# Kernel optimization log

Measured on AMD Instinct MI355X. Metric: run time of the kernel, lower is better.

Reference implementation:

```python
import jax, jax.numpy as jnp
import numpy as np

# dims
B, LP, CIN, AUX = 8, 1024, 64, 32
COUT, OUT_LEN = 64, 512
DM, DI, NS, PH, NH = 1024, 2048, 16, 64, 32  # d_model, d_inner, d_state, headdim, n_heads
NL, PATCH, KPRE, KCONV = 4, 8, 5, 4
GG, KH, CHUNK = 8, 2048, 64  # kan grid, kan hidden, chunk_size
DIN = 2 * DI + 2 * NS + NH   # in_proj output: z, xBC, dt
CONV_DIM = DI + 2 * NS


def _conv1d(x, w, b, stride, pad_l, pad_r, groups=1):
    # x: [B, C, L], w: [O, I/groups, K]
    y = jax.lax.conv_general_dilated(x, w, (stride,), [(pad_l, pad_r)],
                                     dimension_numbers=("NCH", "OIH", "NCH"),
                                     feature_group_count=groups)
    return y + b[None, :, None]


def _rmsnorm(x, w):
    return x * jax.lax.rsqrt(jnp.mean(x * x, axis=-1, keepdims=True) + 1e-5) * w


def _mamba(u, in_w, conv_w, conv_b, A_log, Dh, dt_bias, out_w):
    # Mamba2-style selective SSM block (bias-free projections, causal depthwise conv).
    Bs, L, _ = u.shape
    zxbcdt = jnp.einsum("bld,ed->ble", u, in_w)  # [B,L,DIN]
    z = zxbcdt[..., :DI]
    xBC = zxbcdt[..., DI:DI + CONV_DIM]
    dt = jax.nn.softplus(zxbcdt[..., DI + CONV_DIM:] + dt_bias)  # [B,L,NH]
    xBC = jax.nn.silu(_conv1d(xBC.transpose(0, 2, 1), conv_w, conv_b, 1, KCONV - 1, 0,
                              groups=CONV_DIM)).transpose(0, 2, 1)
    xh = xBC[..., :DI].reshape(Bs, L, NH, PH)
    Bm = xBC[..., DI:DI + NS]   # [B,L,NS]
    Cm = xBC[..., DI + NS:]     # [B,L,NS]
    dA = jnp.exp(-jnp.exp(A_log) * dt)  # [B,L,NH]

    def step(s, t):
        x_t, B_t, C_t, dA_t, dt_t = t
        s = s * dA_t[:, :, None, None] + jnp.einsum("bhp,bn,bh->bhpn", x_t, B_t, dt_t)
        return s, jnp.einsum("bhpn,bn->bhp", s, C_t)

    s0 = jnp.zeros((Bs, NH, PH, NS), u.dtype)
    xs = (xh.transpose(1, 0, 2, 3), Bm.transpose(1, 0, 2), Cm.transpose(1, 0, 2),
          dA.transpose(1, 0, 2), dt.transpose(1, 0, 2))
    _, ys = jax.lax.scan(step, s0, xs)  # ys: [L,B,NH,PH]
    y = ys.transpose(1, 0, 2, 3) + xh * Dh[None, None, :, None]
    y = y.reshape(Bs, L, DI) * jax.nn.silu(z)
    return jnp.einsum("ble,de->bld", y, out_w)


def _kan(x, log_bw, base_w, base_b, spline_w):
    # Gaussian-basis KAN layer: base Linear + spline Linear over RBF expansion.
    grid = jnp.linspace(-2.0, 2.0, GG)
    bw = jnp.exp(log_bw)[None] + 1e-6                 # [1,in,1]
    basis = jnp.exp(-((x[..., None] - grid[None, None, :]) ** 2) / (2.0 * bw * bw))
    return x @ base_w.T + base_b + basis.reshape(x.shape[0], -1) @ spline_w.T


def setup_inputs() -> dict:
    ks = iter(jax.random.split(jax.random.key(0), 64))
    nrm = lambda shape, s=0.02: jax.random.normal(next(ks), shape, jnp.float32) * s
    inp = {"x_prefix": jax.random.normal(next(ks), (B, LP, CIN), jnp.float32),
           "y_aux": jax.random.normal(next(ks), (B, AUX), jnp.float32),
           "pre_conv_w": nrm((DM, CIN, KPRE), 0.1), "pre_conv_b": jnp.zeros((DM,)),
           "patch_w": nrm((DM, DM, PATCH), 0.05), "patch_b": jnp.zeros((DM,))}
    for pre in ("fwd", "bwd"):
        inp[pre + "_norm_w"] = jnp.ones((NL, DM))
        inp[pre + "_in_w"] = nrm((NL, DIN, DM))
        inp[pre + "_conv_w"] = nrm((NL, CONV_DIM, 1, KCONV), 0.1)
        inp[pre + "_conv_b"] = jnp.zeros((NL, CONV_DIM))
        inp[pre + "_A_log"] = jnp.zeros((NL, NH))
        inp[pre + "_D"] = jnp.ones((NL, NH))
        inp[pre + "_dt_bias"] = nrm((NL, NH), 0.5)
        inp[pre + "_out_w"] = nrm((NL, DM, DI))
    inp.update(aux_w=nrm((DM, AUX)), aux_b=jnp.zeros((DM,)),
               kan1_log_bw=jnp.zeros((3 * DM, 1)), kan1_base_w=nrm((KH, 3 * DM)),
               kan1_base_b=jnp.zeros((KH,)), kan1_spline_w=nrm((KH, 3 * DM * GG), 0.005),
               kan2_log_bw=jnp.zeros((KH, 1)), kan2_base_w=nrm((DM, KH)),
               kan2_base_b=jnp.zeros((DM,)), kan2_spline_w=nrm((DM, KH * GG), 0.005),
               shared_w=nrm((DM, DM)), shared_b=jnp.zeros((DM,)),
               heads_w=nrm((COUT, OUT_LEN, DM)), heads_b=jnp.zeros((COUT, OUT_LEN)))
    return inp


def reference(x_prefix, y_aux, pre_conv_w, pre_conv_b, patch_w, patch_b,
              fwd_norm_w, fwd_in_w, fwd_conv_w, fwd_conv_b, fwd_A_log, fwd_D, fwd_dt_bias, fwd_out_w,
              bwd_norm_w, bwd_in_w, bwd_conv_w, bwd_conv_b, bwd_A_log, bwd_D, bwd_dt_bias, bwd_out_w,
              aux_w, aux_b, kan1_log_bw, kan1_base_w, kan1_base_b, kan1_spline_w,
              kan2_log_bw, kan2_base_w, kan2_base_b, kan2_spline_w,
              shared_w, shared_b, heads_w, heads_b):
    # encode_prefix
    x = jax.nn.silu(_conv1d(x_prefix.transpose(0, 2, 1), pre_conv_w, pre_conv_b, 1, KPRE // 2, KPRE // 2))
    x = _conv1d(x, patch_w, patch_b, PATCH, 0, 0).transpose(0, 2, 1)  # [B, 128, DM]
    rem = x.shape[1] % CHUNK
    if rem:
        x = jnp.pad(x, ((0, 0), (0, CHUNK - rem), (0, 0)))
    h_f, h_b = x, x[:, ::-1]
    for i in range(NL):
        h_f = h_f + _mamba(_rmsnorm(h_f, fwd_norm_w[i]), fwd_in_w[i], fwd_conv_w[i], fwd_conv_b[i],
                           fwd_A_log[i], fwd_D[i], fwd_dt_bias[i], fwd_out_w[i])
        h_b = h_b + _mamba(_rmsnorm(h_b, bwd_norm_w[i]), bwd_in_w[i], bwd_conv_w[i], bwd_conv_b[i],
                           bwd_A_log[i], bwd_D[i], bwd_dt_bias[i], bwd_out_w[i])
    ctx = jnp.concatenate([h_f.mean(1), h_b[:, ::-1].mean(1)], axis=-1)  # [B, 2*DM]
    # fusion + heads
    aux = jax.nn.silu(y_aux @ aux_w.T + aux_b)
    fused = jnp.concatenate([ctx, aux], axis=-1)  # [B, 3*DM]
    fused = jax.nn.silu(_kan(fused, kan1_log_bw, kan1_base_w, kan1_base_b, kan1_spline_w))
    fused = jax.nn.silu(_kan(fused, kan2_log_bw, kan2_base_w, kan2_base_b, kan2_spline_w))
    fused = jax.nn.silu(fused @ shared_w.T + shared_b)
    # all channel heads fused into one batched GEMM: [B, OUT_LEN, COUT]
    return jnp.einsum("bd,cld->blc", fused, heads_w) + heads_b.T[None]
```

## Files before the change

kernel.cpp:

```cpp
#include <hip/hip_runtime.h>
#include <hip/hip_bf16.h>
#include <math.h>

#define B_    8
#define LP_   1024
#define CIN_  64
#define DM_   1024
#define DI_   2048
#define NS_   16
#define PH_   64
#define NH_   32
#define NL_   4
#define GG_   8
#define KH_   2048
#define DIN_  4160
#define NPAD_ 4224
#define CONVD_ 2080
#define L_    128
#define R_    1024
#define OUTL_ 512
#define COUT_ 64

typedef __bf16 bf16x8 __attribute__((ext_vector_type(8)));
typedef float f32x4 __attribute__((ext_vector_type(4)));
typedef unsigned short ushort;

__device__ __forceinline__ float silu_f(float x) { return x / (1.0f + expf(-x)); }

__device__ __forceinline__ ushort f2bu(float x) {
    union { __hip_bfloat16 h; ushort u; } c; c.h = __float2bfloat16(x); return c.u;
}
__device__ __forceinline__ float bu2f(ushort u) {
    union { ushort u; __hip_bfloat16 h; } c; c.u = u; return __bfloat162float(c.h);
}

__device__ __forceinline__ void gload_lds16(const void* g, void* l) {
    __builtin_amdgcn_global_load_lds((const __attribute__((address_space(1))) unsigned int*)g,
                                     (__attribute__((address_space(3))) unsigned int*)l, 16, 0, 0);
}

__device__ __forceinline__ float merge2(float a, float b, int mask, int lane) {
    float x = (lane & mask) ? b : a;
    float y = (lane & mask) ? a : b;
    return x + __shfl_xor(y, mask);
}
__device__ __forceinline__ float reduce8(float* a, int lane) {
    float c0 = merge2(a[0], a[1], 1, lane);
    float c1 = merge2(a[2], a[3], 1, lane);
    float c2 = merge2(a[4], a[5], 1, lane);
    float c3 = merge2(a[6], a[7], 1, lane);
    float d0 = merge2(c0, c1, 2, lane);
    float d1 = merge2(c2, c3, 2, lane);
    float e  = merge2(d0, d1, 4, lane);
    e += __shfl_xor(e, 8);
    e += __shfl_xor(e, 16);
    e += __shfl_xor(e, 32);
    return e;
}

__global__ __launch_bounds__(256) void k_pre_im2col(const float* __restrict__ xp, __hip_bfloat16* __restrict__ out) {
    size_t idx = (size_t)blockIdx.x * 256 + threadIdx.x;
    if (idx >= (size_t)8192 * 320) return;
    int kk = (int)(idx % 320); size_t r = idx / 320;
    int l = (int)(r & 1023); int b = (int)(r >> 10);
    int kp = kk >> 6, c = kk & 63;
    int lp = l + kp - 2;
    float v = 0.f;
    if (lp >= 0 && lp < LP_) v = xp[((size_t)b * LP_ + lp) * CIN_ + c];
    out[idx] = __float2bfloat16(v);
}

__global__ __launch_bounds__(256) void k_wpre_T(const float* __restrict__ w, __hip_bfloat16* __restrict__ out) {
    int idx = blockIdx.x * 256 + threadIdx.x;
    if (idx >= DM_ * 320) return;
    int d = idx / 320, kk = idx % 320;
    int kp = kk >> 6, c = kk & 63;
    out[idx] = __float2bfloat16(w[(d * CIN_ + c) * 5 + kp]);
}

__global__ __launch_bounds__(256) void k_wpatch_T(const float* __restrict__ w, __hip_bfloat16* __restrict__ out) {
    size_t idx = (size_t)blockIdx.x * 256 + threadIdx.x;
    if (idx >= (size_t)DM_ * 8192) return;
    int d = (int)(idx >> 13); int kk = (int)(idx & 8191);
    int kp = kk >> 10, din = kk & 1023;
    out[idx] = __float2bfloat16(w[((size_t)d << 13) + din * 8 + kp]);
}

#define CVT_IN_T4  1081344
#define CVT_OUT_T4 524288
__global__ __launch_bounds__(256) void k_cvt_layer(const float* __restrict__ in0, const float* __restrict__ in1,
                                                   const float* __restrict__ o0, const float* __restrict__ o1,
                                                   __hip_bfloat16* __restrict__ wBB, __hip_bfloat16* __restrict__ wOB) {
    int i = blockIdx.x * 256 + threadIdx.x;
    int dir = 0;
    if (i >= CVT_IN_T4 + CVT_OUT_T4) { dir = 1; i -= CVT_IN_T4 + CVT_OUT_T4; }
    const float* inw = dir ? in1 : in0;
    const float* outw = dir ? o1 : o0;
    if (i < CVT_IN_T4) {
        int idx = i * 4; int row = idx >> 10;
        __hip_bfloat16* dst = wBB + (size_t)dir * NPAD_ * 1024 + idx;
        if (row < DIN_) {
            float4 v = *(const float4*)(inw + idx);
            dst[0] = __float2bfloat16(v.x); dst[1] = __float2bfloat16(v.y);
            dst[2] = __float2bfloat16(v.z); dst[3] = __float2bfloat16(v.w);
        } else {
            dst[0] = __float2bfloat16(0.f); dst[1] = __float2bfloat16(0.f);
            dst[2] = __float2bfloat16(0.f); dst[3] = __float2bfloat16(0.f);
        }
    } else {
        int idx = (i - CVT_IN_T4) * 4;
        __hip_bfloat16* dst = wOB + (size_t)dir * 1024 * 2048 + idx;
        float4 v = *(const float4*)(outw + idx);
        dst[0] = __float2bfloat16(v.x); dst[1] = __float2bfloat16(v.y);
        dst[2] = __float2bfloat16(v.z); dst[3] = __float2bfloat16(v.w);
    }
}

template<int BM, int BN>
__global__ __launch_bounds__(256) void k_gemm_mfma(
    const ushort* __restrict__ A, const ushort* __restrict__ B,
    const float* __restrict__ bias, const float* __restrict__ resid,
    float* __restrict__ Cf, __hip_bfloat16* __restrict__ Cb,
    int Kc, int ldk, int ldc, int Nstore, int act, long sA, long sB, long sC)
{
    constexpr int BK = 32;
    constexpr int WM = BM / 2, WN = BN / 2;
    constexpr int MR = WM / 16, NR = WN / 16;
    constexpr int ACH = BM * 4, BCH = BN * 4;
    __shared__ ushort sAs[2][BM * BK];
    __shared__ ushort sBs[2][BN * BK];
    int tid = threadIdx.x;
    int lane = tid & 63, w = tid >> 6;
    int wr = w >> 1, wc = w & 1;
    int z = blockIdx.z;
    int m0 = blockIdx.y * BM, n0 = blockIdx.x * BN;
    int kbase = (act == 2) ? z * Kc : 0;
    const ushort* Az = A + (size_t)(act == 2 ? 0 : z) * sA + kbase;
    const ushort* Bz = B + (size_t)(act == 2 ? 0 : z) * sB + kbase;

    auto STAGE = [&](int buf, int k0) {
        #pragma unroll
        for (int c = tid; c < ACH; c += 256) {
            int row = c >> 2, col = (c & 3) * 8;
            gload_lds16(Az + (size_t)(m0 + row) * ldk + k0 + col, (char*)&sAs[buf][0] + c * 16);
        }
        #pragma unroll
        for (int c = tid; c < BCH; c += 256) {
            int row = c >> 2, col = (c & 3) * 8;
            gload_lds16(Bz + (size_t)(n0 + row) * ldk + k0 + col, (char*)&sBs[buf][0] + c * 16);
        }
    };

    f32x4 acc[MR][NR] = {};
    const int NT = Kc / BK;
    STAGE(0, 0);
    __syncthreads();
    int cur = 0;
    for (int t = 0; t < NT; ++t) {
        if (t + 1 < NT) STAGE(cur ^ 1, (t + 1) * BK);
        bf16x8 af[MR], bfr[NR];
        #pragma unroll
        for (int m = 0; m < MR; ++m)
            af[m] = *(const bf16x8*)&sAs[cur][(wr * WM + m * 16 + (lane & 15)) * BK + (lane >> 4) * 8];
        #pragma unroll
        for (int n = 0; n < NR; ++n)
            bfr[n] = *(const bf16x8*)&sBs[cur][(wc * WN + n * 16 + (lane & 15)) * BK + (lane >> 4) * 8];
        #pragma unroll
        for (int m = 0; m < MR; ++m)
            #pragma unroll
            for (int n = 0; n < NR; ++n)
                acc[m][n] = __builtin_amdgcn_mfma_f32_16x16x32_bf16(af[m], bfr[n], acc[m][n], 0, 0, 0);
        __syncthreads();
        cur ^= 1;
    }
    const float* residz = resid ? resid + (size_t)z * sC : nullptr;
    float* Cfz = Cf ? Cf + (size_t)z * sC : nullptr;
    __hip_bfloat16* Cbz = Cb ? Cb + (size_t)z * sC : nullptr;
    #pragma unroll
    for (int m = 0; m < MR; ++m) {
        int row = m0 + wr * WM + m * 16 + (lane >> 4) * 4;
        #pragma unroll
        for (int n = 0; n < NR; ++n) {
            int col = n0 + wc * WN + n * 16 + (lane & 15);
            if (col < Nstore) {
                float bv = (bias && act != 2) ? bias[col] : 0.f;
                #pragma unroll
                for (int j = 0; j < 4; ++j) {
                    float v = acc[m][n][j] + bv;
                    if (residz) v += residz[(size_t)(row + j) * ldc + col];
                    if (act == 1) v = silu_f(v);
                    if (Cbz) Cbz[(size_t)(row + j) * ldc + col] = __float2bfloat16(v);
                    else     Cfz[(size_t)(row + j) * ldc + col] = v;
                }
            }
        }
    }
}

__global__ __launch_bounds__(256) void k_patch_fin(const float* __restrict__ part, const float* __restrict__ bias,
                                                   float* __restrict__ hf, float* __restrict__ hb) {
    int i4 = blockIdx.x * 256 + threadIdx.x;
    int idx = i4 * 4;
    int r = idx >> 10, c = idx & 1023;
    float4 v = *(const float4*)(part + idx);
    float4 v1 = *(const float4*)(part + 1048576 + idx);
    float4 v2 = *(const float4*)(part + 2097152 + idx);
    float4 v3 = *(const float4*)(part + 3145728 + idx);
    float4 bv = *(const float4*)(bias + c);
    float4 o;
    o.x = v.x + v1.x + v2.x + v3.x + bv.x;
    o.y = v.y + v1.y + v2.y + v3.y + bv.y;
    o.z = v.z + v1.z + v2.z + v3.z + bv.z;
    o.w = v.w + v1.w + v2.w + v3.w + bv.w;
    *(float4*)(hf + idx) = o;
    *(float4*)(hb + (((size_t)(r ^ 127)) << 10) + c) = o;
}

__global__ __launch_bounds__(256) void k_rmsnorm(const float* __restrict__ h, const float* __restrict__ w0,
                                                 const float* __restrict__ w1, __hip_bfloat16* __restrict__ u) {
    int r = blockIdx.x; int t = threadIdx.x;
    const float* w = (r >> 10) ? w1 : w0;
    const float* row = h + (size_t)r * DM_;
    float v[4]; float ss = 0.f;
    #pragma unroll
    for (int i = 0; i < 4; ++i) { v[i] = row[t + 256 * i]; ss += v[i] * v[i]; }
    #pragma unroll
    for (int o = 32; o; o >>= 1) ss += __shfl_xor(ss, o);
    __shared__ float sred[4];
    if ((t & 63) == 0) sred[t >> 6] = ss;
    __syncthreads();
    float tot = sred[0] + sred[1] + sred[2] + sred[3];
    float scale = rsqrtf(tot * (1.0f / DM_) + 1e-5f);
    #pragma unroll
    for (int i = 0; i < 4; ++i)
        u[(size_t)r * DM_ + t + 256 * i] = __float2bfloat16(v[i] * scale * w[t + 256 * i]);
}

__global__ __launch_bounds__(256) void k_dwconv(const __hip_bfloat16* __restrict__ zx,
                                                const float* __restrict__ cw0, const float* __restrict__ cw1,
                                                const float* __restrict__ cb0, const float* __restrict__ cb1,
                                                __hip_bfloat16* __restrict__ xbc) {
    int idx = blockIdx.x * 256 + threadIdx.x;
    if (idx >= 2048 * 520) return;
    int c4 = idx % 520; int r = idx / 520;
    int dir = r >> 10, rl = r & 1023, l = rl & 127;
    const float* cw = (dir ? cw1 : cw0) + c4 * 16;
    const float* cb = (dir ? cb1 : cb0) + c4 * 4;
    const __hip_bfloat16* zxd = zx + (size_t)dir * 1024 * DIN_;
    float4 acc = *(const float4*)cb;
    #pragma unroll
    for (int k = 0; k < 4; ++k) {
        int lp = l - 3 + k;
        if (lp >= 0) {
            ushort4 raw = *(const ushort4*)(zxd + (size_t)(rl - l + lp) * DIN_ + DI_ + c4 * 4);
            acc.x += bu2f(raw.x) * cw[0 * 4 + k];
            acc.y += bu2f(raw.y) * cw[1 * 4 + k];
            acc.z += bu2f(raw.z) * cw[2 * 4 + k];
            acc.w += bu2f(raw.w) * cw[3 * 4 + k];
        }
    }
    ushort4 o;
    o.x = f2bu(silu_f(acc.x)); o.y = f2bu(silu_f(acc.y));
    o.z = f2bu(silu_f(acc.z)); o.w = f2bu(silu_f(acc.w));
    *(ushort4*)(xbc + (size_t)dir * 1024 * CONVD_ + (size_t)rl * CONVD_ + c4 * 4) = o;
}

__global__ __launch_bounds__(256) void k_scan(const __hip_bfloat16* __restrict__ xbc, const __hip_bfloat16* __restrict__ zx,
                                              const float* __restrict__ dtb0, const float* __restrict__ dtb1,
                                              const float* __restrict__ al0, const float* __restrict__ al1,
                                              const float* __restrict__ D0, const float* __restrict__ D1,
                                              __hip_bfloat16* __restrict__ ys) {
    __shared__ float xs[L_ * PH_];
    __shared__ float Bsh[L_ * NS_];
    __shared__ float Csh[L_ * NS_];
    __shared__ float dts[L_];
    __shared__ float dAs[L_];
    int bx = blockIdx.x;
    int dir = bx >> 8, b = (bx >> 5) & 7, h = bx & 31;
    const __hip_bfloat16* xbcd = xbc + (size_t)dir * 1024 * CONVD_;
    const __hip_bfloat16* zxd  = zx  + (size_t)dir * 1024 * DIN_;
    const float* dt_bias = dir ? dtb1 : dtb0;
    const float* A_log   = dir ? al1 : al0;
    const float* Dh      = dir ? D1 : D0;
    __hip_bfloat16* ysd  = ys + (size_t)dir * 1024 * DI_;
    int t = threadIdx.x;
    for (int i = t; i < L_ * PH_; i += 256) {
        int l = i >> 6, p = i & 63;
        xs[i] = __bfloat162float(xbcd[((size_t)(b * L_ + l)) * CONVD_ + h * PH_ + p]);
    }
    for (int i = t; i < L_ * NS_; i += 256) {
        int l = i >> 4, n = i & 15;
        Bsh[i] = __bfloat162float(xbcd[((size_t)(b * L_ + l)) * CONVD_ + DI_ + n]);
        Csh[i] = __bfloat162float(xbcd[((size_t)(b * L_ + l)) * CONVD_ + DI_ + NS_ + n]);
    }
    if (t < L_) {
        float v = __bfloat162float(zxd[((size_t)(b * L_ + t)) * DIN_ + 4128 + h]) + dt_bias[h];
        float sp = v > 20.f ? v : log1pf(expf(v));
        dts[t] = sp;
        dAs[t] = expf(-expf(A_log[h]) * sp);
    }
    __syncthreads();
    int p = t >> 2, n0 = (t & 3) * 4;
    float Dv = Dh[h];
    float s0 = 0.f, s1 = 0.f, s2 = 0.f, s3 = 0.f;
    for (int l = 0; l < L_; ++l) {
        float x = xs[l * 64 + p];
        float dAv = dAs[l];
        float xdt = x * dts[l];
        s0 = s0 * dAv + xdt * Bsh[l * 16 + n0 + 0];
        s1 = s1 * dAv + xdt * Bsh[l * 16 + n0 + 1];
        s2 = s2 * dAv + xdt * Bsh[l * 16 + n0 + 2];
        s3 = s3 * dAv + xdt * Bsh[l * 16 + n0 + 3];
        float cp = s0 * Csh[l * 16 + n0 + 0] + s1 * Csh[l * 16 + n0 + 1]
                 + s2 * Csh[l * 16 + n0 + 2] + s3 * Csh[l * 16 + n0 + 3];
        cp += __shfl_xor(cp, 1);
        cp += __shfl_xor(cp, 2);
        if ((t & 3) == 0) xs[l * 64 + p] = cp + x * Dv;
    }
    __syncthreads();
    for (int i = t; i < L_ * PH_; i += 256) {
        int l = i >> 6, pp = i & 63;
        float z = __bfloat162float(zxd[((size_t)(b * L_ + l)) * DIN_ + h * PH_ + pp]);
        ysd[((size_t)(b * L_ + l)) * DI_ + h * PH_ + pp] = __float2bfloat16(xs[i] * silu_f(z));
    }
}

__global__ __launch_bounds__(256) void k_meanctx(const float* __restrict__ hf, const float* __restrict__ hb,
                                                 float* __restrict__ fused) {
    int b = blockIdx.x, t = threadIdx.x;
    int d = t * 4;
    float4 sf = {0,0,0,0}, sb = {0,0,0,0};
    for (int l = 0; l < L_; ++l) {
        float4 a = *(const float4*)(hf + ((size_t)b * L_ + l) * DM_ + d);
        float4 c = *(const float4*)(hb + ((size_t)b * L_ + l) * DM_ + d);
        sf.x += a.x; sf.y += a.y; sf.z += a.z; sf.w += a.w;
        sb.x += c.x; sb.y += c.y; sb.z += c.z; sb.w += c.w;
    }
    const float s = 1.f / L_;
    float4 o1 = {sf.x*s, sf.y*s, sf.z*s, sf.w*s};
    float4 o2 = {sb.x*s, sb.y*s, sb.z*s, sb.w*s};
    *(float4*)(fused + b * 3072 + d) = o1;
    *(float4*)(fused + b * 3072 + DM_ + d) = o2;
}

__global__ __launch_bounds__(256) void k_aux(const float* __restrict__ y_aux, const float* __restrict__ aux_w,
                                             const float* __restrict__ aux_b, float* __restrict__ fused) {
    int j = blockIdx.x * 256 + threadIdx.x;
    if (j >= DM_) return;
    for (int b = 0; b < B_; ++b) {
        float acc = aux_b[j];
        for (int a = 0; a < 32; ++a) acc += y_aux[b * 32 + a] * aux_w[j * 32 + a];
        fused[b * 3072 + 2 * DM_ + j] = silu_f(acc);
    }
}

__global__ __launch_bounds__(256) void k_basis(const float* __restrict__ x, const float* __restrict__ log_bw,
                                               float* __restrict__ basis, int Din) {
    int idx = blockIdx.x * 256 + threadIdx.x;
    if (idx >= 8 * Din) return;
    int d = idx % Din;
    float xv = x[idx];
    float bw = expf(log_bw[d]) + 1e-6f;
    float inv = 1.0f / (2.0f * bw * bw);
    #pragma unroll
    for (int g = 0; g < GG_; ++g) {
        float gg = -2.0f + g * (4.0f / 7.0f);
        float df = xv - gg;
        basis[(size_t)idx * GG_ + g] = expf(-df * df * inv);
    }
}

template<int MODE>
__global__ __launch_bounds__(256) void k_dotl(const float* __restrict__ W, const float* __restrict__ X,
                                              const float* __restrict__ bias, float* __restrict__ out,
                                              int K, int Dout, int ldx, int nch, int chOff) {
    __shared__ float sX[8][1024];
    int ch = blockIdx.y;
    int k0 = ch * 1024;
    int tid = threadIdx.x;
    for (int i = tid; i < 2048; i += 256) {
        int b = i >> 8, kk = (i & 255) * 4;
        *(float4*)&sX[b][kk] = *(const float4*)(X + (size_t)b * ldx + k0 + kk);
    }
    __syncthreads();
    int wv = tid >> 6, lane = tid & 63;
    int rowBase = blockIdx.x * 32 + wv * 8;
    for (int j = 0; j < 8; ++j) {
        int row = rowBase + j;
        const float* wr = W + (size_t)row * K + k0;
        float acc[8] = {};
        #pragma unroll
        for (int it = 0; it < 4; ++it) {
            int k = it * 256 + lane * 4;
            float4 wvv = *(const float4*)(wr + k);
            #pragma unroll
            for (int b = 0; b < 8; ++b) {
                float4 xv = *(const float4*)&sX[b][k];
                acc[b] += wvv.x * xv.x + wvv.y * xv.y + wvv.z * xv.z + wvv.w * xv.w;
            }
        }
        float e = reduce8(acc, lane);
        if (lane < 8) {
            if (MODE == 0) {
                out[((size_t)row * nch + chOff + ch) * 8 + lane] = e;
            } else if (MODE == 1) {
                out[(size_t)lane * Dout + row] = silu_f(e + bias[row]);
            } else {
                int c = row >> 9, l = row & 511;
                out[((size_t)lane * OUTL_ + l) * COUT_ + c] = e + bias[row];
            }
        }
    }
}

template<int NCH>
__global__ __launch_bounds__(256) void k_dot_fin(const float* __restrict__ partial, const float* __restrict__ base_b,
                                                 float* __restrict__ out, int Dout) {
    int row = blockIdx.x * 256 + threadIdx.x;
    if (row >= Dout) return;
    float bb = base_b[row];
    #pragma unroll
    for (int b = 0; b < 8; ++b) {
        float s = bb;
        #pragma unroll
        for (int c = 0; c < NCH; ++c) s += partial[((size_t)row * NCH + c) * 8 + b];
        out[(size_t)b * Dout + row] = silu_f(s);
    }
}

extern "C" void kernel_launch(void* const* d_in, const int* in_sizes, int n_in,
                              void* d_out, int out_size, void* d_ws, size_t ws_size,
                              hipStream_t stream) {
    const float* x_prefix = (const float*)d_in[0];
    const float* y_aux    = (const float*)d_in[1];
    const float* pre_w    = (const float*)d_in[2];
    const float* pre_b    = (const float*)d_in[3];
    const float* patch_w  = (const float*)d_in[4];
    const float* patch_b  = (const float*)d_in[5];
    const float* norm_w[2] = {(const float*)d_in[6],  (const float*)d_in[14]};
    const float* in_w[2]   = {(const float*)d_in[7],  (const float*)d_in[15]};
    const float* conv_w[2] = {(const float*)d_in[8],  (const float*)d_in[16]};
    const float* conv_b[2] = {(const float*)d_in[9],  (const float*)d_in[17]};
    const float* A_log[2]  = {(const float*)d_in[10], (const float*)d_in[18]};
    const float* Dvec[2]   = {(const float*)d_in[11], (const float*)d_in[19]};
    const float* dt_b[2]   = {(const float*)d_in[12], (const float*)d_in[20]};
    const float* out_w[2]  = {(const float*)d_in[13], (const float*)d_in[21]};
    const float* aux_w = (const float*)d_in[22];
    const float* aux_b = (const float*)d_in[23];
    const float* k1_lbw = (const float*)d_in[24];
    const float* k1_bw  = (const float*)d_in[25];
    const float* k1_bb  = (const float*)d_in[26];
    const float* k1_sw  = (const float*)d_in[27];
    const float* k2_lbw = (const float*)d_in[28];
    const float* k2_bw  = (const float*)d_in[29];
    const float* k2_bb  = (const float*)d_in[30];
    const float* k2_sw  = (const float*)d_in[31];
    const float* sh_w = (const float*)d_in[32];
    const float* sh_b = (const float*)d_in[33];
    const float* hw   = (const float*)d_in[34];
    const float* hbias= (const float*)d_in[35];
    float* ws = (float*)d_ws;
    float* out = (float*)d_out;

    const size_t o_ApreB   = 0;
    const size_t o_wpreTB  = 1310720;
    const size_t o_x1B     = 1474560;
    const size_t o_wpatchTB= 5668864;
    const size_t o_ppart   = 9863168;
    const size_t o_uB   = 0;
    const size_t o_zxB  = 1048576;
    const size_t o_xbcB = 5308416;
    const size_t o_ysB  = 7438336;
    const size_t o_wBB  = 9535488;
    const size_t o_wOB  = 13860864;
    const size_t o_hf   = 15958016;
    const size_t o_hb   = 17006592;
    const size_t total_f = 18055168;
    const size_t o_f1   = 0;
    const size_t o_bas1 = 24576;
    const size_t o_k1   = 221184;
    const size_t o_bas2 = 237568;
    const size_t o_k2   = 368640;
    const size_t o_f4   = 376832;
    const size_t o_part = 385024;
    if (ws_size < total_f * sizeof(float)) return;

    __hip_bfloat16* ApreB   = (__hip_bfloat16*)(ws + o_ApreB);
    __hip_bfloat16* wpreTB  = (__hip_bfloat16*)(ws + o_wpreTB);
    __hip_bfloat16* x1B     = (__hip_bfloat16*)(ws + o_x1B);
    __hip_bfloat16* wpatchTB= (__hip_bfloat16*)(ws + o_wpatchTB);
    __hip_bfloat16* uB      = (__hip_bfloat16*)(ws + o_uB);
    __hip_bfloat16* zxB     = (__hip_bfloat16*)(ws + o_zxB);
    __hip_bfloat16* xbcB    = (__hip_bfloat16*)(ws + o_xbcB);
    __hip_bfloat16* ysB     = (__hip_bfloat16*)(ws + o_ysB);
    __hip_bfloat16* wBB     = (__hip_bfloat16*)(ws + o_wBB);
    __hip_bfloat16* wOB     = (__hip_bfloat16*)(ws + o_wOB);
    float* hf = ws + o_hf;
    float* hb = ws + o_hb;

    k_wpre_T<<<1280, 256, 0, stream>>>(pre_w, wpreTB);
    k_wpatch_T<<<32768, 256, 0, stream>>>(patch_w, wpatchTB);
    k_pre_im2col<<<10240, 256, 0, stream>>>(x_prefix, ApreB);
    k_gemm_mfma<128,128><<<dim3(8, 64, 1), 256, 0, stream>>>(
        (const ushort*)ApreB, (const ushort*)wpreTB, pre_b, nullptr, nullptr, x1B,
        320, 320, 1024, 1024, 1, 0, 0, 0);
    k_gemm_mfma<64,64><<<dim3(16, 16, 4), 256, 0, stream>>>(
        (const ushort*)x1B, (const ushort*)wpatchTB, nullptr, nullptr, ws + o_ppart, nullptr,
        2048, 8192, 1024, 1024, 2, 0, 0, (long)1024 * 1024);
    k_patch_fin<<<1024, 256, 0, stream>>>(ws + o_ppart, patch_b, hf, hb);

    for (int i = 0; i < NL_; ++i) {
        k_rmsnorm<<<2048, 256, 0, stream>>>(hf, norm_w[0] + (size_t)i * DM_, norm_w[1] + (size_t)i * DM_, uB);
        k_cvt_layer<<<12544, 256, 0, stream>>>(
            in_w[0] + (size_t)i * DIN_ * DM_, in_w[1] + (size_t)i * DIN_ * DM_,
            out_w[0] + (size_t)i * DM_ * DI_, out_w[1] + (size_t)i * DM_ * DI_, wBB, wOB);
        k_gemm_mfma<128,128><<<dim3(33, 8, 2), 256, 0, stream>>>(
            (const ushort*)uB, (const ushort*)wBB, nullptr, nullptr, nullptr, zxB,
            1024, 1024, DIN_, DIN_, 0, (long)1024 * 1024, (long)NPAD_ * 1024, (long)1024 * DIN_);
        k_dwconv<<<4160, 256, 0, stream>>>(zxB,
            conv_w[0] + (size_t)i * CONVD_ * 4, conv_w[1] + (size_t)i * CONVD_ * 4,
            conv_b[0] + (size_t)i * CONVD_, conv_b[1] + (size_t)i * CONVD_, xbcB);
        k_scan<<<512, 256, 0, stream>>>(xbcB, zxB,
            dt_b[0] + i * NH_, dt_b[1] + i * NH_, A_log[0] + i * NH_, A_log[1] + i * NH_,
            Dvec[0] + i * NH_, Dvec[1] + i * NH_, ysB);
        k_gemm_mfma<64,64><<<dim3(16, 16, 2), 256, 0, stream>>>(
            (const ushort*)ysB, (const ushort*)wOB, nullptr, hf, hf, nullptr,
            2048, 2048, 1024, 1024, 0, (long)1024 * 2048, (long)1024 * 2048, (long)1024 * 1024);
    }

    k_meanctx<<<8, 256, 0, stream>>>(hf, hb, ws + o_f1);
    k_aux<<<4, 256, 0, stream>>>(y_aux, aux_w, aux_b, ws + o_f1);
    k_basis<<<96, 256, 0, stream>>>(ws + o_f1, k1_lbw, ws + o_bas1, 3072);
    k_dotl<0><<<dim3(64, 24), 256, 0, stream>>>(k1_sw, ws + o_bas1, nullptr, ws + o_part, 24576, 2048, 24576, 27, 0);
    k_dotl<0><<<dim3(64, 3),  256, 0, stream>>>(k1_bw, ws + o_f1,   nullptr, ws + o_part, 3072,  2048, 3072,  27, 24);
    k_dot_fin<27><<<8, 256, 0, stream>>>(ws + o_part, k1_bb, ws + o_k1, 2048);
    k_basis<<<64, 256, 0, stream>>>(ws + o_k1, k2_lbw, ws + o_bas2, 2048);
    k_dotl<0><<<dim3(32, 16), 256, 0, stream>>>(k2_sw, ws + o_bas2, nullptr, ws + o_part, 16384, 1024, 16384, 18, 0);
    k_dotl<0><<<dim3(32, 2),  256, 0, stream>>>(k2_bw, ws + o_k1,   nullptr, ws + o_part, 2048,  1024, 2048,  18, 16);
    k_dot_fin<18><<<4, 256, 0, stream>>>(ws + o_part, k2_bb, ws + o_k2, 1024);
    k_dotl<1><<<dim3(32, 1), 256, 0, stream>>>(sh_w, ws + o_k2, sh_b, ws + o_f4, 1024, 1024, 1024, 1, 0);
    k_dotl<2><<<dim3(1024, 1), 256, 0, stream>>>(hw, ws + o_f4, hbias, out, 1024, 32768, 1024, 1, 0);
}
```

Before: 966.9 us.

## Fuse depthwise conv into scan, split-K out-proj and patch GEMMs, parallelize meanctx

The depthwise causal conv plus SiLU is now computed inside the scan kernel straight from the in_proj output, which removes the xbc intermediate buffer and a kernel launch. The patch GEMM and the per-layer out-projection GEMM move to 128x128 tiles with split-K (8 and 4 splits), writing partial sums that small finalize kernels reduce, and the out-projection finalize also adds the residual. The mean-context kernel is spread over 64 blocks with a shared-memory reduction instead of 8 blocks. The trade-off is extra partial-sum traffic and an extra reduction launch per layer in exchange for more parallelism and larger MFMA tiles. The conv inputs are also re-read redundantly for each head.

```diff
diff --git a/kernel.cpp b/kernel.cpp
--- a/kernel.cpp
+++ b/kernel.cpp
@@ -119,9 +119,10 @@
 template<int BM, int BN>
 __global__ __launch_bounds__(256) void k_gemm_mfma(
     const ushort* __restrict__ A, const ushort* __restrict__ B,
-    const float* __restrict__ bias, const float* __restrict__ resid,
+    const float* __restrict__ bias,
     float* __restrict__ Cf, __hip_bfloat16* __restrict__ Cb,
-    int Kc, int ldk, int ldc, int Nstore, int act, long sA, long sB, long sC)
+    int Kc, int ldk, int ldc, int Nstore, int act, int nsplit,
+    long sA, long sB, long sC)
 {
     constexpr int BK = 32;
     constexpr int WM = BM / 2, WN = BN / 2;
@@ -133,10 +134,11 @@
     int lane = tid & 63, w = tid >> 6;
     int wr = w >> 1, wc = w & 1;
     int z = blockIdx.z;
+    int dir = z / nsplit, ks = z - dir * nsplit;
+    int kbase = ks * Kc;
     int m0 = blockIdx.y * BM, n0 = blockIdx.x * BN;
-    int kbase = (act == 2) ? z * Kc : 0;
-    const ushort* Az = A + (size_t)(act == 2 ? 0 : z) * sA + kbase;
-    const ushort* Bz = B + (size_t)(act == 2 ? 0 : z) * sB + kbase;
+    const ushort* Az = A + (size_t)dir * sA + kbase;
+    const ushort* Bz = B + (size_t)dir * sB + kbase;
 
     auto STAGE = [&](int buf, int k0) {
         #pragma unroll
@@ -173,9 +175,6 @@
         __syncthreads();
         cur ^= 1;
     }
-    const float* residz = resid ? resid + (size_t)z * sC : nullptr;
-    float* Cfz = Cf ? Cf + (size_t)z * sC : nullptr;
-    __hip_bfloat16* Cbz = Cb ? Cb + (size_t)z * sC : nullptr;
     #pragma unroll
     for (int m = 0; m < MR; ++m) {
         int row = m0 + wr * WM + m * 16 + (lane >> 4) * 4;
@@ -183,14 +182,20 @@
         for (int n = 0; n < NR; ++n) {
             int col = n0 + wc * WN + n * 16 + (lane & 15);
             if (col < Nstore) {
-                float bv = (bias && act != 2) ? bias[col] : 0.f;
-                #pragma unroll
-                for (int j = 0; j < 4; ++j) {
-                    float v = acc[m][n][j] + bv;
-                    if (residz) v += residz[(size_t)(row + j) * ldc + col];
-                    if (act == 1) v = silu_f(v);
-                    if (Cbz) Cbz[(size_t)(row + j) * ldc + col] = __float2bfloat16(v);
-                    else     Cfz[(size_t)(row + j) * ldc + col] = v;
+                if (act == 2) {
+                    float* Cfz = Cf + (size_t)z * sC;
+                    #pragma unroll
+                    for (int j = 0; j < 4; ++j)
+                        Cfz[(size_t)(row + j) * ldc + col] = acc[m][n][j];
+                } else {
+                    __hip_bfloat16* Cbz = Cb + (size_t)dir * sC;
+                    float bv = bias ? bias[col] : 0.f;
+                    #pragma unroll
+                    for (int j = 0; j < 4; ++j) {
+                        float v = acc[m][n][j] + bv;
+                        if (act == 1) v = silu_f(v);
+                        Cbz[(size_t)(row + j) * ldc + col] = __float2bfloat16(v);
+                    }
                 }
             }
         }
@@ -202,18 +207,30 @@
     int i4 = blockIdx.x * 256 + threadIdx.x;
     int idx = i4 * 4;
     int r = idx >> 10, c = idx & 1023;
-    float4 v = *(const float4*)(part + idx);
-    float4 v1 = *(const float4*)(part + 1048576 + idx);
-    float4 v2 = *(const float4*)(part + 2097152 + idx);
-    float4 v3 = *(const float4*)(part + 3145728 + idx);
     float4 bv = *(const float4*)(bias + c);
-    float4 o;
-    o.x = v.x + v1.x + v2.x + v3.x + bv.x;
-    o.y = v.y + v1.y + v2.y + v3.y + bv.y;
-    o.z = v.z + v1.z + v2.z + v3.z + bv.z;
-    o.w = v.w + v1.w + v2.w + v3.w + bv.w;
+    float4 o = bv;
+    #pragma unroll
+    for (int s = 0; s < 8; ++s) {
+        float4 v = *(const float4*)(part + (size_t)s * 1048576 + idx);
+        o.x += v.x; o.y += v.y; o.z += v.z; o.w += v.w;
+    }
     *(float4*)(hf + idx) = o;
     *(float4*)(hb + (((size_t)(r ^ 127)) << 10) + c) = o;
+}
+
+__global__ __launch_bounds__(256) void k_oproj_fin(const float* __restrict__ part, float* __restrict__ h) {
+    int i4 = blockIdx.x * 256 + threadIdx.x;
+    int idx = i4 * 4;
+    int dir = idx >> 20;
+    int off = idx & 1048575;
+    const float* p = part + (size_t)dir * 4 * 1048576 + off;
+    float4 o = *(const float4*)(h + idx);
+    #pragma unroll
+    for (int s = 0; s < 4; ++s) {
+        float4 v = *(const float4*)(p + (size_t)s * 1048576);
+        o.x += v.x; o.y += v.y; o.z += v.z; o.w += v.w;
+    }
+    *(float4*)(h + idx) = o;
 }
 
 __global__ __launch_bounds__(256) void k_rmsnorm(const float* __restrict__ h, const float* __restrict__ w0,
@@ -236,36 +253,9 @@
         u[(size_t)r * DM_ + t + 256 * i] = __float2bfloat16(v[i] * scale * w[t + 256 * i]);
 }
 
-__global__ __launch_bounds__(256) void k_dwconv(const __hip_bfloat16* __restrict__ zx,
-                                                const float* __restrict__ cw0, const float* __restrict__ cw1,
-                                                const float* __restrict__ cb0, const float* __restrict__ cb1,
-                                                __hip_bfloat16* __restrict__ xbc) {
-    int idx = blockIdx.x * 256 + threadIdx.x;
-    if (idx >= 2048 * 520) return;
-    int c4 = idx % 520; int r = idx / 520;
-    int dir = r >> 10, rl = r & 1023, l = rl & 127;
-    const float* cw = (dir ? cw1 : cw0) + c4 * 16;
-    const float* cb = (dir ? cb1 : cb0) + c4 * 4;
-    const __hip_bfloat16* zxd = zx + (size_t)dir * 1024 * DIN_;
-    float4 acc = *(const float4*)cb;
-    #pragma unroll
-    for (int k = 0; k < 4; ++k) {
-        int lp = l - 3 + k;
-        if (lp >= 0) {
-            ushort4 raw = *(const ushort4*)(zxd + (size_t)(rl - l + lp) * DIN_ + DI_ + c4 * 4);
-            acc.x += bu2f(raw.x) * cw[0 * 4 + k];
-            acc.y += bu2f(raw.y) * cw[1 * 4 + k];
-            acc.z += bu2f(raw.z) * cw[2 * 4 + k];
-            acc.w += bu2f(raw.w) * cw[3 * 4 + k];
-        }
-    }
-    ushort4 o;
-    o.x = f2bu(silu_f(acc.x)); o.y = f2bu(silu_f(acc.y));
-    o.z = f2bu(silu_f(acc.z)); o.w = f2bu(silu_f(acc.w));
-    *(ushort4*)(xbc + (size_t)dir * 1024 * CONVD_ + (size_t)rl * CONVD_ + c4 * 4) = o;
-}
-
-__global__ __launch_bounds__(256) void k_scan(const __hip_bfloat16* __restrict__ xbc, const __hip_bfloat16* __restrict__ zx,
+__global__ __launch_bounds__(256) void k_scan(const __hip_bfloat16* __restrict__ zx,
+                                              const float* __restrict__ cw0, const float* __restrict__ cw1,
+                                              const float* __restrict__ cb0, const float* __restrict__ cb1,
                                               const float* __restrict__ dtb0, const float* __restrict__ dtb1,
                                               const float* __restrict__ al0, const float* __restrict__ al1,
                                               const float* __restrict__ D0, const float* __restrict__ D1,
@@ -277,24 +267,58 @@
     __shared__ float dAs[L_];
     int bx = blockIdx.x;
     int dir = bx >> 8, b = (bx >> 5) & 7, h = bx & 31;
-    const __hip_bfloat16* xbcd = xbc + (size_t)dir * 1024 * CONVD_;
-    const __hip_bfloat16* zxd  = zx  + (size_t)dir * 1024 * DIN_;
+    const __hip_bfloat16* zxd = zx + (size_t)dir * 1024 * DIN_;
+    const float* cw = dir ? cw1 : cw0;
+    const float* cb = dir ? cb1 : cb0;
     const float* dt_bias = dir ? dtb1 : dtb0;
     const float* A_log   = dir ? al1 : al0;
     const float* Dh      = dir ? D1 : D0;
     __hip_bfloat16* ysd  = ys + (size_t)dir * 1024 * DI_;
     int t = threadIdx.x;
-    for (int i = t; i < L_ * PH_; i += 256) {
-        int l = i >> 6, p = i & 63;
-        xs[i] = __bfloat162float(xbcd[((size_t)(b * L_ + l)) * CONVD_ + h * PH_ + p]);
-    }
-    for (int i = t; i < L_ * NS_; i += 256) {
-        int l = i >> 4, n = i & 15;
-        Bsh[i] = __bfloat162float(xbcd[((size_t)(b * L_ + l)) * CONVD_ + DI_ + n]);
-        Csh[i] = __bfloat162float(xbcd[((size_t)(b * L_ + l)) * CONVD_ + DI_ + NS_ + n]);
+    for (int i = t; i < 2048; i += 256) {
+        int l = i >> 4, p4 = i & 15;
+        int cc = h * PH_ + p4 * 4;
+        float a0 = cb[cc + 0], a1 = cb[cc + 1], a2 = cb[cc + 2], a3 = cb[cc + 3];
+        #pragma unroll
+        for (int k = 0; k < 4; ++k) {
+            int lp = l - 3 + k;
+            if (lp >= 0) {
+                ushort4 raw = *(const ushort4*)(zxd + (size_t)(b * L_ + lp) * DIN_ + DI_ + cc);
+                a0 += bu2f(raw.x) * cw[(cc + 0) * 4 + k];
+                a1 += bu2f(raw.y) * cw[(cc + 1) * 4 + k];
+                a2 += bu2f(raw.z) * cw[(cc + 2) * 4 + k];
+                a3 += bu2f(raw.w) * cw[(cc + 3) * 4 + k];
+            }
+        }
+        float* xp = &xs[l * PH_ + p4 * 4];
+        xp[0] = silu_f(a0); xp[1] = silu_f(a1); xp[2] = silu_f(a2); xp[3] = silu_f(a3);
+    }
+    for (int i = t; i < 1024; i += 256) {
+        int l = i >> 3, q4 = i & 7;
+        int cc = DI_ + q4 * 4;
+        float a0 = cb[cc + 0], a1 = cb[cc + 1], a2 = cb[cc + 2], a3 = cb[cc + 3];
+        #pragma unroll
+        for (int k = 0; k < 4; ++k) {
+            int lp = l - 3 + k;
+            if (lp >= 0) {
+                ushort4 raw = *(const ushort4*)(zxd + (size_t)(b * L_ + lp) * DIN_ + DI_ + cc);
+                a0 += bu2f(raw.x) * cw[(cc + 0) * 4 + k];
+                a1 += bu2f(raw.y) * cw[(cc + 1) * 4 + k];
+                a2 += bu2f(raw.z) * cw[(cc + 2) * 4 + k];
+                a3 += bu2f(raw.w) * cw[(cc + 3) * 4 + k];
+            }
+        }
+        float r0 = silu_f(a0), r1 = silu_f(a1), r2 = silu_f(a2), r3 = silu_f(a3);
+        if (q4 < 4) {
+            float* bp = &Bsh[l * NS_ + q4 * 4];
+            bp[0] = r0; bp[1] = r1; bp[2] = r2; bp[3] = r3;
+        } else {
+            float* cp = &Csh[l * NS_ + (q4 - 4) * 4];
+            cp[0] = r0; cp[1] = r1; cp[2] = r2; cp[3] = r3;
+        }
     }
     if (t < L_) {
-        float v = __bfloat162float(zxd[((size_t)(b * L_ + t)) * DIN_ + 4128 + h]) + dt_bias[h];
+        float v = bu2f(*(const ushort*)(zxd + (size_t)(b * L_ + t) * DIN_ + 4128 + h)) + dt_bias[h];
         float sp = v > 20.f ? v : log1pf(expf(v));
         dts[t] = sp;
         dAs[t] = expf(-expf(A_log[h]) * sp);
@@ -320,27 +344,35 @@
     __syncthreads();
     for (int i = t; i < L_ * PH_; i += 256) {
         int l = i >> 6, pp = i & 63;
-        float z = __bfloat162float(zxd[((size_t)(b * L_ + l)) * DIN_ + h * PH_ + pp]);
+        float z = bu2f(*(const ushort*)(zxd + (size_t)(b * L_ + l) * DIN_ + h * PH_ + pp));
         ysd[((size_t)(b * L_ + l)) * DI_ + h * PH_ + pp] = __float2bfloat16(xs[i] * silu_f(z));
     }
 }
 
 __global__ __launch_bounds__(256) void k_meanctx(const float* __restrict__ hf, const float* __restrict__ hb,
                                                  float* __restrict__ fused) {
-    int b = blockIdx.x, t = threadIdx.x;
-    int d = t * 4;
+    int b = blockIdx.x >> 3, ch = blockIdx.x & 7;
+    int t = threadIdx.x;
+    int d4 = t & 31, lg = t >> 5;
+    int d = ch * 128 + d4 * 4;
     float4 sf = {0,0,0,0}, sb = {0,0,0,0};
-    for (int l = 0; l < L_; ++l) {
+    for (int l = lg; l < L_; l += 8) {
         float4 a = *(const float4*)(hf + ((size_t)b * L_ + l) * DM_ + d);
         float4 c = *(const float4*)(hb + ((size_t)b * L_ + l) * DM_ + d);
         sf.x += a.x; sf.y += a.y; sf.z += a.z; sf.w += a.w;
         sb.x += c.x; sb.y += c.y; sb.z += c.z; sb.w += c.w;
     }
-    const float s = 1.f / L_;
-    float4 o1 = {sf.x*s, sf.y*s, sf.z*s, sf.w*s};
-    float4 o2 = {sb.x*s, sb.y*s, sb.z*s, sb.w*s};
-    *(float4*)(fused + b * 3072 + d) = o1;
-    *(float4*)(fused + b * 3072 + DM_ + d) = o2;
+    __shared__ float rf[8][128], rb[8][128];
+    *(float4*)&rf[lg][d4 * 4] = sf;
+    *(float4*)&rb[lg][d4 * 4] = sb;
+    __syncthreads();
+    if (t < 128) {
+        float s1 = 0.f, s2 = 0.f;
+        #pragma unroll
+        for (int g = 0; g < 8; ++g) { s1 += rf[g][t]; s2 += rb[g][t]; }
+        fused[b * 3072 + ch * 128 + t] = s1 * (1.f / L_);
+        fused[b * 3072 + DM_ + ch * 128 + t] = s2 * (1.f / L_);
+    }
 }
 
 __global__ __launch_bounds__(256) void k_aux(const float* __restrict__ y_aux, const float* __restrict__ aux_w,
@@ -466,16 +498,15 @@
     const size_t o_wpreTB  = 1310720;
     const size_t o_x1B     = 1474560;
     const size_t o_wpatchTB= 5668864;
-    const size_t o_ppart   = 9863168;
     const size_t o_uB   = 0;
     const size_t o_zxB  = 1048576;
-    const size_t o_xbcB = 5308416;
-    const size_t o_ysB  = 7438336;
-    const size_t o_wBB  = 9535488;
-    const size_t o_wOB  = 13860864;
-    const size_t o_hf   = 15958016;
-    const size_t o_hb   = 17006592;
-    const size_t total_f = 18055168;
+    const size_t o_ysB  = 5308416;
+    const size_t o_wBB  = 7405568;
+    const size_t o_wOB  = 11730944;
+    const size_t o_hf   = 13828096;
+    const size_t o_hb   = 14876672;
+    const size_t o_spart= 15925248;
+    const size_t total_f = 24313856;
     const size_t o_f1   = 0;
     const size_t o_bas1 = 24576;
     const size_t o_k1   = 221184;
@@ -491,7 +522,6 @@
     __hip_bfloat16* wpatchTB= (__hip_bfloat16*)(ws + o_wpatchTB);
     __hip_bfloat16* uB      = (__hip_bfloat16*)(ws + o_uB);
     __hip_bfloat16* zxB     = (__hip_bfloat16*)(ws + o_zxB);
-    __hip_bfloat16* xbcB    = (__hip_bfloat16*)(ws + o_xbcB);
     __hip_bfloat16* ysB     = (__hip_bfloat16*)(ws + o_ysB);
     __hip_bfloat16* wBB     = (__hip_bfloat16*)(ws + o_wBB);
     __hip_bfloat16* wOB     = (__hip_bfloat16*)(ws + o_wOB);
@@ -502,12 +532,12 @@
     k_wpatch_T<<<32768, 256, 0, stream>>>(patch_w, wpatchTB);
     k_pre_im2col<<<10240, 256, 0, stream>>>(x_prefix, ApreB);
     k_gemm_mfma<128,128><<<dim3(8, 64, 1), 256, 0, stream>>>(
-        (const ushort*)ApreB, (const ushort*)wpreTB, pre_b, nullptr, nullptr, x1B,
-        320, 320, 1024, 1024, 1, 0, 0, 0);
-    k_gemm_mfma<64,64><<<dim3(16, 16, 4), 256, 0, stream>>>(
-        (const ushort*)x1B, (const ushort*)wpatchTB, nullptr, nullptr, ws + o_ppart, nullptr,
-        2048, 8192, 1024, 1024, 2, 0, 0, (long)1024 * 1024);
-    k_patch_fin<<<1024, 256, 0, stream>>>(ws + o_ppart, patch_b, hf, hb);
+        (const ushort*)ApreB, (const ushort*)wpreTB, pre_b, nullptr, x1B,
+        320, 320, 1024, 1024, 1, 1, 0, 0, 0);
+    k_gemm_mfma<128,128><<<dim3(8, 8, 8), 256, 0, stream>>>(
+        (const ushort*)x1B, (const ushort*)wpatchTB, nullptr, ws + o_spart, nullptr,
+        1024, 8192, 1024, 1024, 2, 8, 0, 0, (long)1024 * 1024);
+    k_patch_fin<<<1024, 256, 0, stream>>>(ws + o_spart, patch_b, hf, hb);
 
     for (int i = 0; i < NL_; ++i) {
         k_rmsnorm<<<2048, 256, 0, stream>>>(hf, norm_w[0] + (size_t)i * DM_, norm_w[1] + (size_t)i * DM_, uB);
@@ -515,20 +545,20 @@
             in_w[0] + (size_t)i * DIN_ * DM_, in_w[1] + (size_t)i * DIN_ * DM_,
             out_w[0] + (size_t)i * DM_ * DI_, out_w[1] + (size_t)i * DM_ * DI_, wBB, wOB);
         k_gemm_mfma<128,128><<<dim3(33, 8, 2), 256, 0, stream>>>(
-            (const ushort*)uB, (const ushort*)wBB, nullptr, nullptr, nullptr, zxB,
-            1024, 1024, DIN_, DIN_, 0, (long)1024 * 1024, (long)NPAD_ * 1024, (long)1024 * DIN_);
-        k_dwconv<<<4160, 256, 0, stream>>>(zxB,
+            (const ushort*)uB, (const ushort*)wBB, nullptr, nullptr, zxB,
+            1024, 1024, DIN_, DIN_, 0, 1, (long)1024 * 1024, (long)NPAD_ * 1024, (long)1024 * DIN_);
+        k_scan<<<512, 256, 0, stream>>>(zxB,
             conv_w[0] + (size_t)i * CONVD_ * 4, conv_w[1] + (size_t)i * CONVD_ * 4,
-            conv_b[0] + (size_t)i * CONVD_, conv_b[1] + (size_t)i * CONVD_, xbcB);
-        k_scan<<<512, 256, 0, stream>>>(xbcB, zxB,
+            conv_b[0] + (size_t)i * CONVD_, conv_b[1] + (size_t)i * CONVD_,
             dt_b[0] + i * NH_, dt_b[1] + i * NH_, A_log[0] + i * NH_, A_log[1] + i * NH_,
             Dvec[0] + i * NH_, Dvec[1] + i * NH_, ysB);
-        k_gemm_mfma<64,64><<<dim3(16, 16, 2), 256, 0, stream>>>(
-            (const ushort*)ysB, (const ushort*)wOB, nullptr, hf, hf, nullptr,
-            2048, 2048, 1024, 1024, 0, (long)1024 * 2048, (long)1024 * 2048, (long)1024 * 1024);
-    }
-
-    k_meanctx<<<8, 256, 0, stream>>>(hf, hb, ws + o_f1);
+        k_gemm_mfma<128,128><<<dim3(8, 8, 8), 256, 0, stream>>>(
+            (const ushort*)ysB, (const ushort*)wOB, nullptr, ws + o_spart, nullptr,
+            512, 2048, 1024, 1024, 2, 4, (long)1024 * 2048, (long)1024 * 2048, (long)1024 * 1024);
+        k_oproj_fin<<<2048, 256, 0, stream>>>(ws + o_spart, hf);
+    }
+
+    k_meanctx<<<64, 256, 0, stream>>>(hf, hb, ws + o_f1);
     k_aux<<<4, 256, 0, stream>>>(y_aux, aux_w, aux_b, ws + o_f1);
     k_basis<<<96, 256, 0, stream>>>(ws + o_f1, k1_lbw, ws + o_bas1, 3072);
     k_dotl<0><<<dim3(64, 24), 256, 0, stream>>>(k1_sw, ws + o_bas1, nullptr, ws + o_part, 24576, 2048, 24576, 27, 0);
```

After: 918.7 us. -5.0%, faster.
